# Kernel optimization log

Measured on AMD Instinct MI355X. Metric: run time of the kernel, lower is better.

## Reference

```python
import jax, jax.numpy as jnp
import numpy as np

EPS = 1e-5
HID = 32
FUSED = 33 * 33 * 33  # 35937


def _subnet(x, gamma, beta, W1, b1, W2, b2, W3, b3):
    # BatchNorm1d in training mode: batch mean / biased variance
    mu = jnp.mean(x, axis=0)
    var = jnp.mean((x - mu) ** 2, axis=0)
    xn = (x - mu) / jnp.sqrt(var + EPS) * gamma + beta
    h = jax.nn.relu(xn @ W1 + b1)
    h = jax.nn.relu(h @ W2 + b2)
    return jax.nn.relu(h @ W3 + b3)


def _subnet_params(key, in_dim):
    ks = jax.random.split(key, 6)
    s_in = 1.0 / np.sqrt(in_dim)
    s_h = 1.0 / np.sqrt(HID)
    return dict(
        gamma=jnp.ones((in_dim,), jnp.float32),
        beta=jnp.zeros((in_dim,), jnp.float32),
        W1=jax.random.uniform(ks[0], (in_dim, HID), jnp.float32, -s_in, s_in),
        b1=jax.random.uniform(ks[1], (HID,), jnp.float32, -s_in, s_in),
        W2=jax.random.uniform(ks[2], (HID, HID), jnp.float32, -s_h, s_h),
        b2=jax.random.uniform(ks[3], (HID,), jnp.float32, -s_h, s_h),
        W3=jax.random.uniform(ks[4], (HID, HID), jnp.float32, -s_h, s_h),
        b3=jax.random.uniform(ks[5], (HID,), jnp.float32, -s_h, s_h),
    )


def setup_inputs() -> dict:
    key = jax.random.key(0)
    ks = jax.random.split(key, 10)
    B = 8192
    inp = {
        'US_x': jax.random.normal(ks[0], (B, 1024), jnp.float32),
        'CDFI_x': jax.random.normal(ks[1], (B, 1024), jnp.float32),
        'marker_x': jax.random.normal(ks[2], (B, 10), jnp.float32),
    }
    for pref, k, d in (('us', ks[3], 1024), ('cd', ks[4], 1024), ('mk', ks[5], 10)):
        for n, v in _subnet_params(k, d).items():
            inp[f'{pref}_{n}'] = v
    s1 = 1.0 / np.sqrt(FUSED)
    s2 = 1.0 / np.sqrt(33)
    inp['Wf1'] = jax.random.uniform(ks[6], (FUSED, 33), jnp.float32, -s1, s1)
    inp['bf1'] = jax.random.uniform(ks[7], (33,), jnp.float32, -s1, s1)
    inp['Wf2'] = jax.random.uniform(ks[8], (33, 5), jnp.float32, -s2, s2)
    inp['bf2'] = jax.random.uniform(ks[9], (5,), jnp.float32, -s2, s2)
    return inp


def reference(US_x, CDFI_x, marker_x,
              us_gamma, us_beta, us_W1, us_b1, us_W2, us_b2, us_W3, us_b3,
              cd_gamma, cd_beta, cd_W1, cd_b1, cd_W2, cd_b2, cd_W3, cd_b3,
              mk_gamma, mk_beta, mk_W1, mk_b1, mk_W2, mk_b2, mk_W3, mk_b3,
              Wf1, bf1, Wf2, bf2):
    B = US_x.shape[0]
    us_h = _subnet(US_x, us_gamma, us_beta, us_W1, us_b1, us_W2, us_b2, us_W3, us_b3)
    cd_h = _subnet(CDFI_x, cd_gamma, cd_beta, cd_W1, cd_b1, cd_W2, cd_b2, cd_W3, cd_b3)
    mk_h = _subnet(marker_x, mk_gamma, mk_beta, mk_W1, mk_b1, mk_W2, mk_b2, mk_W3, mk_b3)
    ones = jnp.ones((B, 1), jnp.float32)
    us1 = jnp.concatenate([ones, us_h], axis=1)   # [B,33]
    cd1 = jnp.concatenate([ones, cd_h], axis=1)   # [B,33]
    mk1 = jnp.concatenate([ones, mk_h], axis=1)   # [B,33]
    # fused[b,k,j,i] = mk1[b,k] * cd1[b,j] * us1[b,i]; flattened row-major
    fused = jnp.einsum('bk,bj,bi->bkji', mk1, cd1, us1).reshape(B, FUSED)
    h = jax.nn.relu(fused @ Wf1 + bf1)
    return jax.nn.sigmoid(h @ Wf2 + bf2)
```

## Files before the change

kernel.cpp:

```cpp
#include <hip/hip_runtime.h>
#include <hip/hip_bf16.h>
#include <math.h>

typedef __hip_bfloat16 bf16;
typedef __attribute__((ext_vector_type(4))) float f32x4;
typedef __attribute__((ext_vector_type(8))) short s16x8;

#define NB 8192
#define KP 1152
#define NP 1152
#define NKT 18
#define SBLK 256

struct SubP {
    const float* x; const float* gamma; const float* beta;
    const float* W1; const float* b1; const float* W2; const float* b2;
    const float* W3; const float* b3;
    float* sum; float* sumsq; float* a; float* b1p; float* hout;
    int F;
};
struct SubP3 { SubP s[3]; };

__global__ void __launch_bounds__(256) stats3_kernel(SubP3 P) {
    const SubP p = P.s[blockIdx.z];
    int t = threadIdx.x;
    int blk = blockIdx.x;
    int row0 = blk * 32;
    if (p.F == 1024) {
        f32x4 s = {0.f, 0.f, 0.f, 0.f}, s2 = {0.f, 0.f, 0.f, 0.f};
        const float* xp = p.x + (size_t)row0 * 1024 + t * 4;
        #pragma unroll 8
        for (int r = 0; r < 32; r++) {
            f32x4 v = *(const f32x4*)(xp + (size_t)r * 1024);
            s += v; s2 += v * v;
        }
        int f = t * 4;
        *(f32x4*)&p.sum[(size_t)blk * 2048 + f]   = s;
        *(f32x4*)&p.sumsq[(size_t)blk * 2048 + f] = s2;
    } else {
        __shared__ float ls[16], ls2[16];
        if (t < 16) { ls[t] = 0.f; ls2[t] = 0.f; }
        __syncthreads();
        int F = p.F;
        for (int idx = t; idx < 32 * F; idx += 256) {
            float v = p.x[(size_t)row0 * F + idx];
            int f = idx % 10;
            atomicAdd(&ls[f], v);
            atomicAdd(&ls2[f], v * v);
        }
        __syncthreads();
        if (t < F) {
            p.sum[(size_t)blk * 2048 + t]   = ls[t];
            p.sumsq[(size_t)blk * 2048 + t] = ls2[t];
        }
    }
}

__global__ void prep3_kernel(SubP3 P) {
    const SubP p = P.s[blockIdx.y];
    int f0 = blockIdx.x * 32;
    if (f0 >= p.F) return;
    int t = threadIdx.x;
    __shared__ float c_sh[32];
    __shared__ float red[8][33];
    __shared__ float rs[8][33], rs2[8][33];
    int fc = p.F - f0; if (fc > 32) fc = 32;
    int fi = t & 31, g = t >> 5;
    {
        float s = 0.f, s2 = 0.f;
        if (fi < fc) {
            for (int blk = g; blk < SBLK; blk += 8) {
                s  += p.sum[(size_t)blk * 2048 + f0 + fi];
                s2 += p.sumsq[(size_t)blk * 2048 + f0 + fi];
            }
        }
        rs[g][fi] = s; rs2[g][fi] = s2;
    }
    __syncthreads();
    if (t < 32) {
        float c = 0.f;
        if (t < fc) {
            float sm = 0.f, sq = 0.f;
            #pragma unroll
            for (int gg = 0; gg < 8; gg++) { sm += rs[gg][t]; sq += rs2[gg][t]; }
            int f = f0 + t;
            float mu  = sm * (1.f / 8192.f);
            float var = sq * (1.f / 8192.f) - mu * mu;
            float a = p.gamma[f] * rsqrtf(var + 1e-5f);
            p.a[f] = a;
            c = p.beta[f] - mu * a;
        }
        c_sh[t] = c;
    }
    __syncthreads();
    int h = t & 31; g = t >> 5;
    float s = 0.f;
    for (int fi2 = g; fi2 < fc; fi2 += 8)
        s += c_sh[fi2] * p.W1[(size_t)(f0 + fi2) * 32 + h];
    red[g][h] = s;
    __syncthreads();
    if (t < 32) {
        float tot = 0.f;
        #pragma unroll
        for (int gg = 0; gg < 8; gg++) tot += red[gg][t];
        atomicAdd(&p.b1p[t], tot);
    }
}

__global__ void __launch_bounds__(256) subnet3_kernel(SubP3 P) {
    const SubP p = P.s[blockIdx.y];
    const int F = p.F;
    __shared__ float smem[8832];
    float* Red = smem;
    float* H1  = smem + 3456;
    float* W23 = smem + 4608;
    float* H2  = smem;

    int t = threadIdx.x;
    int row0 = blockIdx.x * 32;
    int kg = t >> 6;
    int lane = t & 63;
    int hg = lane & 7, h0 = hg * 4;
    int rg = (lane >> 3) & 3;
    int ks = lane >> 5;

    float acc[4][8] = {};

    if (F == 1024) {
        float* Xt = smem;
        float* Wt = smem + 4224;
        int xr = t >> 3, xc = (t & 7) * 16;
        int wk = t >> 1, wh = (t & 1) * 16;
        const float* xbase = p.x + (size_t)row0 * 1024;
        f32x4 xp[4], wp[4]; float av;
        #pragma unroll
        for (int i = 0; i < 4; i++) xp[i] = *(const f32x4*)&xbase[(size_t)xr * 1024 + xc + i * 4];
        #pragma unroll
        for (int i = 0; i < 4; i++) wp[i] = *(const f32x4*)&p.W1[(size_t)wk * 32 + wh + i * 4];
        av = p.a[wk];
        int kb = (kg * 2 + ks) * 16;
        for (int c = 0; c < 8; c++) {
            __syncthreads();
            #pragma unroll
            for (int i = 0; i < 4; i++) *(f32x4*)&Xt[xr * 132 + xc + i * 4] = xp[i];
            #pragma unroll
            for (int i = 0; i < 4; i++) *(f32x4*)&Wt[wk * 36 + wh + i * 4] = wp[i] * av;
            if (c < 7) {
                int k0 = (c + 1) * 128;
                #pragma unroll
                for (int i = 0; i < 4; i++) xp[i] = *(const f32x4*)&xbase[(size_t)xr * 1024 + k0 + xc + i * 4];
                #pragma unroll
                for (int i = 0; i < 4; i++) wp[i] = *(const f32x4*)&p.W1[(size_t)(k0 + wk) * 32 + wh + i * 4];
                av = p.a[k0 + wk];
            }
            __syncthreads();
            #pragma unroll
            for (int s = 0; s < 4; s++) {
                int kk = kb + s * 4;
                f32x4 wv[4], xv[8];
                #pragma unroll
                for (int j = 0; j < 4; j++)  wv[j]  = *(const f32x4*)&Wt[(kk + j) * 36 + h0];
                #pragma unroll
                for (int ri = 0; ri < 8; ri++) xv[ri] = *(const f32x4*)&Xt[(rg + 4 * ri) * 132 + kk];
                #pragma unroll
                for (int j = 0; j < 4; j++)
                    #pragma unroll
                    for (int hi = 0; hi < 4; hi++) {
                        float w = wv[j][hi];
                        #pragma unroll
                        for (int ri = 0; ri < 8; ri++)
                            acc[hi][ri] = fmaf(w, xv[ri][j], acc[hi][ri]);
                    }
            }
        }
    } else {
        float* Xt = smem;
        float* Wt = smem + 2176;
        int kbase = (kg * 2 + ks) * 8;
        for (int k0 = 0; k0 < F; k0 += 64) {
            int kc = F - k0; if (kc > 64) kc = 64;
            int kcp = (kc + 3) & ~3;
            __syncthreads();
            for (int idx = t; idx < 32 * kcp; idx += 256) {
                int r = idx / kcp, kk = idx - r * kcp;
                Xt[r * 68 + kk] = (kk < kc) ? p.x[(size_t)(row0 + r) * F + k0 + kk] : 0.f;
            }
            for (int idx = t; idx < kcp * 32; idx += 256) {
                int kk = idx >> 5, hh = idx & 31;
                Wt[kk * 36 + hh] = (kk < kc) ? p.a[k0 + kk] * p.W1[(size_t)(k0 + kk) * 32 + hh] : 0.f;
            }
            __syncthreads();
            #pragma unroll
            for (int s = 0; s < 2; s++) {
                int kk = kbase + s * 4;
                if (kk < kcp) {
                    f32x4 wv[4], xv[8];
                    #pragma unroll
                    for (int j = 0; j < 4; j++)  wv[j]  = *(const f32x4*)&Wt[(kk + j) * 36 + h0];
                    #pragma unroll
                    for (int ri = 0; ri < 8; ri++) xv[ri] = *(const f32x4*)&Xt[(rg + 4 * ri) * 68 + kk];
                    #pragma unroll
                    for (int j = 0; j < 4; j++)
                        #pragma unroll
                        for (int hi = 0; hi < 4; hi++) {
                            float w = wv[j][hi];
                            #pragma unroll
                            for (int ri = 0; ri < 8; ri++)
                                acc[hi][ri] = fmaf(w, xv[ri][j], acc[hi][ri]);
                        }
                }
            }
        }
    }
    #pragma unroll
    for (int hi = 0; hi < 4; hi++)
        #pragma unroll
        for (int ri = 0; ri < 8; ri++)
            acc[hi][ri] += __shfl_xor(acc[hi][ri], 32);
    __syncthreads();
    if (kg > 0 && ks == 0) {
        #pragma unroll
        for (int ri = 0; ri < 8; ri++) {
            int r = rg + 4 * ri;
            f32x4 v = {acc[0][ri], acc[1][ri], acc[2][ri], acc[3][ri]};
            *(f32x4*)&Red[(kg - 1) * 1152 + r * 36 + h0] = v;
        }
    }
    for (int idx = t; idx < 1024; idx += 256) W23[(idx >> 5) * 33 + (idx & 31)] = p.W2[idx];
    __syncthreads();
    if (kg == 0 && ks == 0) {
        f32x4 b;
        #pragma unroll
        for (int hi = 0; hi < 4; hi++) b[hi] = p.b1[h0 + hi] + p.b1p[h0 + hi];
        #pragma unroll
        for (int ri = 0; ri < 8; ri++) {
            int r = rg + 4 * ri;
            f32x4 v = {acc[0][ri], acc[1][ri], acc[2][ri], acc[3][ri]};
            #pragma unroll
            for (int pp = 0; pp < 3; pp++)
                v += *(const f32x4*)&Red[pp * 1152 + r * 36 + h0];
            v += b;
            #pragma unroll
            for (int hi = 0; hi < 4; hi++)
                H1[r * 36 + h0 + hi] = fmaxf(v[hi], 0.f);
        }
    }
    __syncthreads();
    int h = t & 31, rq = t >> 5;
    {
        float a2[4] = {};
        for (int q = 0; q < 32; q++) {
            float w = W23[q * 33 + h];
            #pragma unroll
            for (int i = 0; i < 4; i++) a2[i] += H1[(rq * 4 + i) * 36 + q] * w;
        }
        float bv = p.b2[h];
        #pragma unroll
        for (int i = 0; i < 4; i++) H2[(rq * 4 + i) * 36 + h] = fmaxf(a2[i] + bv, 0.f);
    }
    __syncthreads();
    for (int idx = t; idx < 1024; idx += 256) W23[(idx >> 5) * 33 + (idx & 31)] = p.W3[idx];
    __syncthreads();
    {
        float a3[4] = {};
        for (int q = 0; q < 32; q++) {
            float w = W23[q * 33 + h];
            #pragma unroll
            for (int i = 0; i < 4; i++) a3[i] += H2[(rq * 4 + i) * 36 + q] * w;
        }
        float bv = p.b3[h];
        #pragma unroll
        for (int i = 0; i < 4; i++)
            p.hout[(size_t)(row0 + rq * 4 + i) * 32 + h] = fmaxf(a3[i] + bv, 0.f);
    }
}

__global__ void __launch_bounds__(256) build_both(const float* __restrict__ mk_h,
                           const float* __restrict__ us_h,
                           bf16* __restrict__ p1,
                           const float* __restrict__ Wf1, bf16* __restrict__ W2t) {
    int blk = blockIdx.x;
    int t = threadIdx.x;
    if (blk < NB / 4) {
        int r = t >> 6, lane = t & 63;
        int b = blk * 4 + r;
        __shared__ float mk1[4][34], us1[4][34];
        if (lane == 0) { mk1[r][0] = 1.f; us1[r][0] = 1.f; }
        if (lane < 32) mk1[r][lane + 1] = mk_h[(size_t)b * 32 + lane];
        else           us1[r][lane - 31] = us_h[(size_t)b * 32 + (lane - 32)];
        __syncthreads();
        #pragma unroll
        for (int c = 0; c < 3; c++) {
            int chunk = lane + 64 * c;
            if (chunk < 144) {
                int base = chunk * 8;
                s16x8 v;
                #pragma unroll
                for (int e = 0; e < 8; e++) {
                    int idx = base + e;
                    float val = 0.f;
                    if (idx < 1089) {
                        int k = idx / 33, i = idx - k * 33;
                        val = mk1[r][k] * us1[r][i];
                    }
                    __hip_bfloat16 hb = __float2bfloat16(val);
                    v[e] = *(short*)&hb;
                }
                *(s16x8*)(p1 + (size_t)b * KP + base) = v;
            }
        }
    } else {
        int kj = blk - NB / 4;
        int k = kj / 33, j = kj - k * 33;
        __shared__ float tile[1089];
        const float* src = Wf1 + (size_t)k * 35937 + (size_t)j * 1089;
        for (int idx = t; idx < 1089; idx += 256) tile[idx] = src[idx];
        __syncthreads();
        for (int idx = t; idx < 1089; idx += 256) {
            int o = idx / 33, i = idx - o * 33;
            W2t[(size_t)(j * 33 + o) * KP + k * 33 + i] = __float2bfloat16(tile[i * 33 + o]);
        }
        if (k == 0) {
            bf16 z = __float2bfloat16(0.f);
            for (int idx = t; idx < 33 * 63; idx += 256) {
                int o = idx / 63, kkp = 1089 + idx - o * 63;
                W2t[(size_t)(j * 33 + o) * KP + kkp] = z;
            }
        }
    }
}

__global__ void __launch_bounds__(512) gemm_kernel(const bf16* __restrict__ A,
                                                   const bf16* __restrict__ Bt,
                                                   bf16* __restrict__ S) {
    __shared__ __align__(16) bf16 As[2][256 * 64];
    __shared__ __align__(16) bf16 Bs[2][192 * 64];
    int t = threadIdx.x;
    int wv = t >> 6, lane = t & 63;
    int m0 = blockIdx.x * 256;
    int n0 = blockIdx.y * 144;
    int fr = lane & 15;
    int q  = lane >> 4;
    int lr8 = lane >> 3;
    int sslot = (lane & 7) ^ lr8;

    const bf16* Ag = A  + (size_t)(m0 + wv * 32 + lr8) * KP + sslot * 8;
    const bf16* Bg = Bt + (size_t)(n0 + wv * 24 + lr8) * KP + sslot * 8;

    f32x4 acc[2][9] = {};

    auto stageA = [&](int buf, int T) {
        bf16* Ad = &As[buf][wv * 32 * 64];
        const bf16* s = Ag + T * 64;
        #pragma unroll
        for (int i = 0; i < 4; i++)
            __builtin_amdgcn_global_load_lds(
                (const __attribute__((address_space(1))) void*)(s + (size_t)i * 8 * KP),
                (__attribute__((address_space(3))) void*)(Ad + i * 512), 16, 0, 0);
    };
    auto stageB = [&](int buf, int T) {
        bf16* Bd = &Bs[buf][wv * 24 * 64];
        const bf16* s = Bg + T * 64;
        #pragma unroll
        for (int c = 0; c < 3; c++)
            __builtin_amdgcn_global_load_lds(
                (const __attribute__((address_space(1))) void*)(s + (size_t)c * 8 * KP),
                (__attribute__((address_space(3))) void*)(Bd + c * 512), 16, 0, 0);
    };

    stageA(0, 0);
    stageB(0, 0);

    for (int T = 0; T < NKT; T++) {
        int b = T & 1;
        const bf16* Ab = &As[b][0];
        const bf16* Bb = &Bs[b][0];
        if (T < NKT - 1) {
            stageA(b ^ 1, T + 1);
            asm volatile("s_waitcnt vmcnt(4)" ::: "memory");
        } else {
            asm volatile("s_waitcnt vmcnt(0)" ::: "memory");
        }
        __builtin_amdgcn_s_barrier();
        asm volatile("" ::: "memory");
        {
            int sl = (q ^ (fr & 7)) * 8;
            s16x8 af0 = *(const s16x8*)(Ab + (wv * 32 + fr) * 64 + sl);
            s16x8 af1 = *(const s16x8*)(Ab + (wv * 32 + 16 + fr) * 64 + sl);
            s16x8 bfv[9];
            #pragma unroll
            for (int n2 = 0; n2 < 9; n2++)
                bfv[n2] = *(const s16x8*)(Bb + (n2 * 16 + fr) * 64 + sl);
            __builtin_amdgcn_s_setprio(1);
            #pragma unroll
            for (int n2 = 0; n2 < 9; n2++) {
                acc[0][n2] = __builtin_amdgcn_mfma_f32_16x16x32_bf16(af0, bfv[n2], acc[0][n2], 0, 0, 0);
                acc[1][n2] = __builtin_amdgcn_mfma_f32_16x16x32_bf16(af1, bfv[n2], acc[1][n2], 0, 0, 0);
            }
            __builtin_amdgcn_s_setprio(0);
        }
        if (T < NKT - 1) stageB(b ^ 1, T + 1);
        {
            int sl = ((4 + q) ^ (fr & 7)) * 8;
            s16x8 af0 = *(const s16x8*)(Ab + (wv * 32 + fr) * 64 + sl);
            s16x8 af1 = *(const s16x8*)(Ab + (wv * 32 + 16 + fr) * 64 + sl);
            s16x8 bfv[9];
            #pragma unroll
            for (int n2 = 0; n2 < 9; n2++)
                bfv[n2] = *(const s16x8*)(Bb + (n2 * 16 + fr) * 64 + sl);
            __builtin_amdgcn_s_setprio(1);
            #pragma unroll
            for (int n2 = 0; n2 < 9; n2++) {
                acc[0][n2] = __builtin_amdgcn_mfma_f32_16x16x32_bf16(af0, bfv[n2], acc[0][n2], 0, 0, 0);
                acc[1][n2] = __builtin_amdgcn_mfma_f32_16x16x32_bf16(af1, bfv[n2], acc[1][n2], 0, 0, 0);
            }
            __builtin_amdgcn_s_setprio(0);
        }
        asm volatile("s_waitcnt lgkmcnt(0)" ::: "memory");
        __builtin_amdgcn_sched_barrier(0);
        __builtin_amdgcn_s_barrier();
        asm volatile("" ::: "memory");
    }

    int col = lane & 15, rowg = (lane >> 4) * 4;
    #pragma unroll
    for (int mt = 0; mt < 2; mt++)
        #pragma unroll
        for (int n2 = 0; n2 < 9; n2++)
            #pragma unroll
            for (int r = 0; r < 4; r++) {
                int gr = m0 + wv * 32 + mt * 16 + rowg + r;
                int gc = n0 + n2 * 16 + col;
                S[(size_t)gr * NP + gc] = __float2bfloat16(acc[mt][n2][r]);
            }
}

__global__ void __launch_bounds__(256) epilogue_kernel(const bf16* __restrict__ S,
                                const float* __restrict__ cd_h,
                                const float* __restrict__ bf1, const float* __restrict__ Wf2,
                                const float* __restrict__ bf2, float* __restrict__ out) {
    int w = threadIdx.x >> 6;
    int lane = threadIdx.x & 63;
    int b = blockIdx.x * 4 + w;
    __shared__ __align__(16) unsigned short Sl[4][1152];
    __shared__ float cdsh[4][33];
    __shared__ float hsh[4][40];
    const bf16* Srow = S + (size_t)b * NP;
    #pragma unroll
    for (int pass = 0; pass < 3; pass++) {
        int idx = lane + pass * 64;
        if (idx < 144)
            *(s16x8*)&Sl[w][idx * 8] = *(const s16x8*)(Srow + idx * 8);
    }
    if (lane == 0) cdsh[w][0] = 1.f;
    if (lane < 32) cdsh[w][lane + 1] = cd_h[(size_t)b * 32 + lane];
    __syncthreads();
    if (lane < 33) {
        float acc = bf1[lane];
        #pragma unroll 3
        for (int j = 0; j < 33; j++) {
            unsigned short sv = Sl[w][j * 33 + lane];
            acc += cdsh[w][j] * __bfloat162float(*(bf16*)&sv);
        }
        hsh[w][lane] = fmaxf(acc, 0.f);
    }
    __syncthreads();
    if (lane < 5) {
        float o = bf2[lane];
        for (int q = 0; q < 33; q++) o += hsh[w][q] * Wf2[q * 5 + lane];
        out[(size_t)b * 5 + lane] = 1.f / (1.f + expf(-o));
    }
}

extern "C" void kernel_launch(void* const* d_in, const int* in_sizes, int n_in,
                              void* d_out, int out_size, void* d_ws, size_t ws_size,
                              hipStream_t stream) {
    const float* US_x     = (const float*)d_in[0];
    const float* CDFI_x   = (const float*)d_in[1];
    const float* marker_x = (const float*)d_in[2];
    const float* Wf1      = (const float*)d_in[27];
    const float* bf1      = (const float*)d_in[28];
    const float* Wf2      = (const float*)d_in[29];
    const float* bf2      = (const float*)d_in[30];
    float* out = (float*)d_out;

    char* ws = (char*)d_ws;
    size_t off = 0;
    auto alloc = [&](size_t bytes) -> void* {
        void* p = ws + off;
        off = (off + bytes + 255) & ~(size_t)255;
        return p;
    };

    float* b1p_buf  = (float*)alloc(3 * 128 * sizeof(float));
    float* pstat    = (float*)alloc((size_t)3 * SBLK * 2048 * sizeof(float));
    float* a_buf[3], *h_buf[3];
    for (int i = 0; i < 3; i++) {
        a_buf[i] = (float*)alloc(1024 * 4);
        h_buf[i] = (float*)alloc((size_t)NB * 32 * 4);
    }
    bf16*  p1   = (bf16*)alloc((size_t)NB * KP * 2);
    bf16*  W2t  = (bf16*)alloc((size_t)NP * KP * 2);
    bf16*  S    = (bf16*)alloc((size_t)NB * NP * 2);

    SubP3 P;
    const float* xs[3] = {US_x, CDFI_x, marker_x};
    int Fs[3] = {1024, 1024, 10};
    for (int i = 0; i < 3; i++) {
        int base = 3 + i * 8;
        P.s[i].x     = xs[i];
        P.s[i].gamma = (const float*)d_in[base + 0];
        P.s[i].beta  = (const float*)d_in[base + 1];
        P.s[i].W1    = (const float*)d_in[base + 2];
        P.s[i].b1    = (const float*)d_in[base + 3];
        P.s[i].W2    = (const float*)d_in[base + 4];
        P.s[i].b2    = (const float*)d_in[base + 5];
        P.s[i].W3    = (const float*)d_in[base + 6];
        P.s[i].b3    = (const float*)d_in[base + 7];
        P.s[i].sum   = pstat + (size_t)i * SBLK * 2048;
        P.s[i].sumsq = pstat + (size_t)i * SBLK * 2048 + 1024;
        P.s[i].b1p   = b1p_buf + i * 128;
        P.s[i].a     = a_buf[i];
        P.s[i].hout  = h_buf[i];
        P.s[i].F     = Fs[i];
    }

    float* us_h = h_buf[0];
    float* cd_h = h_buf[1];
    float* mk_h = h_buf[2];

    hipMemsetAsync(b1p_buf, 0, 3 * 128 * sizeof(float), stream);

    stats3_kernel<<<dim3(SBLK, 1, 3), 256, 0, stream>>>(P);
    prep3_kernel<<<dim3(32, 3), 256, 0, stream>>>(P);
    subnet3_kernel<<<dim3(256, 3), 256, 0, stream>>>(P);

    build_both<<<NB / 4 + 1089, 256, 0, stream>>>(mk_h, us_h, p1, Wf1, W2t);

    gemm_kernel<<<dim3(NB / 256, NP / 144), 512, 0, stream>>>(p1, W2t, S);

    epilogue_kernel<<<NB / 4, 256, 0, stream>>>(S, cd_h, bf1, Wf2, bf2, out);
}
```

Baseline: 246.4 us.

## Use bf16 MFMA for subnet first layer with pre-scaled transposed W1

The prep kernel now writes a transposed, BN-scale-folded bf16 copy of W1 for the 1024-wide subnets. The subnet kernel stages X (converted to bf16) and that W1 copy into swizzled LDS and runs the first-layer matmul with 16x16x32 bf16 MFMA instructions, replacing the fp32 FMA loop. It also reorganizes the cross-wave reduction. This removes scalar FMA work but lowers the precision of the first layer to bf16 inputs.

```diff
diff --git a/kernel.cpp b/kernel.cpp
--- a/kernel.cpp
+++ b/kernel.cpp
@@ -17,6 +17,7 @@
     const float* W1; const float* b1; const float* W2; const float* b2;
     const float* W3; const float* b3;
     float* sum; float* sumsq; float* a; float* b1p; float* hout;
+    bf16* w1t;
     int F;
 };
 struct SubP3 { SubP s[3]; };
@@ -62,6 +63,7 @@
     if (f0 >= p.F) return;
     int t = threadIdx.x;
     __shared__ float c_sh[32];
+    __shared__ float ash[32];
     __shared__ float red[8][33];
     __shared__ float rs[8][33], rs2[8][33];
     int fc = p.F - f0; if (fc > 32) fc = 32;
@@ -78,7 +80,7 @@
     }
     __syncthreads();
     if (t < 32) {
-        float c = 0.f;
+        float c = 0.f, av = 0.f;
         if (t < fc) {
             float sm = 0.f, sq = 0.f;
             #pragma unroll
@@ -86,11 +88,11 @@
             int f = f0 + t;
             float mu  = sm * (1.f / 8192.f);
             float var = sq * (1.f / 8192.f) - mu * mu;
-            float a = p.gamma[f] * rsqrtf(var + 1e-5f);
-            p.a[f] = a;
-            c = p.beta[f] - mu * a;
-        }
-        c_sh[t] = c;
+            av = p.gamma[f] * rsqrtf(var + 1e-5f);
+            p.a[f] = av;
+            c = p.beta[f] - mu * av;
+        }
+        c_sh[t] = c; ash[t] = av;
     }
     __syncthreads();
     int h = t & 31; g = t >> 5;
@@ -105,12 +107,19 @@
         for (int gg = 0; gg < 8; gg++) tot += red[gg][t];
         atomicAdd(&p.b1p[t], tot);
     }
+    if (p.F == 1024) {
+        for (int idx = t; idx < 1024; idx += 256) {
+            int kk = idx >> 5, hh = idx & 31;
+            p.w1t[(size_t)hh * 1024 + f0 + kk] =
+                __float2bfloat16(ash[kk] * p.W1[(size_t)(f0 + kk) * 32 + hh]);
+        }
+    }
 }
 
 __global__ void __launch_bounds__(256) subnet3_kernel(SubP3 P) {
     const SubP p = P.s[blockIdx.y];
     const int F = p.F;
-    __shared__ float smem[8832];
+    __shared__ float smem[9760];
     float* Red = smem;
     float* H1  = smem + 3456;
     float* W23 = smem + 4608;
@@ -124,58 +133,105 @@
     int rg = (lane >> 3) & 3;
     int ks = lane >> 5;
 
-    float acc[4][8] = {};
-
     if (F == 1024) {
-        float* Xt = smem;
-        float* Wt = smem + 4224;
+        bf16* Xl = (bf16*)(smem + 5664);
+        bf16* Wl = (bf16*)(smem + 7712);
         int xr = t >> 3, xc = (t & 7) * 16;
-        int wk = t >> 1, wh = (t & 1) * 16;
-        const float* xbase = p.x + (size_t)row0 * 1024;
-        f32x4 xp[4], wp[4]; float av;
-        #pragma unroll
-        for (int i = 0; i < 4; i++) xp[i] = *(const f32x4*)&xbase[(size_t)xr * 1024 + xc + i * 4];
-        #pragma unroll
-        for (int i = 0; i < 4; i++) wp[i] = *(const f32x4*)&p.W1[(size_t)wk * 32 + wh + i * 4];
-        av = p.a[wk];
-        int kb = (kg * 2 + ks) * 16;
+        int sw = xr & 7;
+        int s0 = ((t & 7) * 2) ^ sw, s1 = ((t & 7) * 2 + 1) ^ sw;
+        const float* xbase = p.x + (size_t)(row0 + xr) * 1024 + xc;
+        const bf16*  wbase = p.w1t + (size_t)xr * 1024 + xc;
+        f32x4 xp[4]; s16x8 wp0, wp1;
+        #pragma unroll
+        for (int i = 0; i < 4; i++) xp[i] = *(const f32x4*)(xbase + i * 4);
+        wp0 = *(const s16x8*)(wbase);
+        wp1 = *(const s16x8*)(wbase + 8);
+
+        f32x4 acc[2][2] = {};
+        int fr = lane & 15, qq = lane >> 4;
+        int rsw0 = fr & 7;
+
         for (int c = 0; c < 8; c++) {
-            __syncthreads();
-            #pragma unroll
-            for (int i = 0; i < 4; i++) *(f32x4*)&Xt[xr * 132 + xc + i * 4] = xp[i];
-            #pragma unroll
-            for (int i = 0; i < 4; i++) *(f32x4*)&Wt[wk * 36 + wh + i * 4] = wp[i] * av;
+            __builtin_amdgcn_s_barrier();
+            asm volatile("" ::: "memory");
+            {
+                s16x8 v0, v1;
+                #pragma unroll
+                for (int i = 0; i < 2; i++)
+                    #pragma unroll
+                    for (int e = 0; e < 4; e++) {
+                        __hip_bfloat16 hb = __float2bfloat16(xp[i][e]);
+                        v0[i * 4 + e] = *(short*)&hb;
+                    }
+                #pragma unroll
+                for (int i = 0; i < 2; i++)
+                    #pragma unroll
+                    for (int e = 0; e < 4; e++) {
+                        __hip_bfloat16 hb = __float2bfloat16(xp[2 + i][e]);
+                        v1[i * 4 + e] = *(short*)&hb;
+                    }
+                *(s16x8*)((char*)Xl + xr * 256 + s0 * 16) = v0;
+                *(s16x8*)((char*)Xl + xr * 256 + s1 * 16) = v1;
+                *(s16x8*)((char*)Wl + xr * 256 + s0 * 16) = wp0;
+                *(s16x8*)((char*)Wl + xr * 256 + s1 * 16) = wp1;
+            }
             if (c < 7) {
                 int k0 = (c + 1) * 128;
                 #pragma unroll
-                for (int i = 0; i < 4; i++) xp[i] = *(const f32x4*)&xbase[(size_t)xr * 1024 + k0 + xc + i * 4];
-                #pragma unroll
-                for (int i = 0; i < 4; i++) wp[i] = *(const f32x4*)&p.W1[(size_t)(k0 + wk) * 32 + wh + i * 4];
-                av = p.a[k0 + wk];
-            }
-            __syncthreads();
-            #pragma unroll
-            for (int s = 0; s < 4; s++) {
-                int kk = kb + s * 4;
-                f32x4 wv[4], xv[8];
-                #pragma unroll
-                for (int j = 0; j < 4; j++)  wv[j]  = *(const f32x4*)&Wt[(kk + j) * 36 + h0];
-                #pragma unroll
-                for (int ri = 0; ri < 8; ri++) xv[ri] = *(const f32x4*)&Xt[(rg + 4 * ri) * 132 + kk];
-                #pragma unroll
-                for (int j = 0; j < 4; j++)
+                for (int i = 0; i < 4; i++) xp[i] = *(const f32x4*)(xbase + k0 + i * 4);
+                wp0 = *(const s16x8*)(wbase + k0);
+                wp1 = *(const s16x8*)(wbase + k0 + 8);
+            }
+            asm volatile("s_waitcnt lgkmcnt(0)" ::: "memory");
+            __builtin_amdgcn_sched_barrier(0);
+            __builtin_amdgcn_s_barrier();
+            asm volatile("" ::: "memory");
+            {
+                int sx = kg * 4 + qq;
+                int sl = (sx ^ rsw0) * 16;
+                s16x8 a0 = *(const s16x8*)((char*)Xl + fr * 256 + sl);
+                s16x8 a1 = *(const s16x8*)((char*)Xl + (16 + fr) * 256 + sl);
+                s16x8 b0 = *(const s16x8*)((char*)Wl + fr * 256 + sl);
+                s16x8 b1 = *(const s16x8*)((char*)Wl + (16 + fr) * 256 + sl);
+                acc[0][0] = __builtin_amdgcn_mfma_f32_16x16x32_bf16(a0, b0, acc[0][0], 0, 0, 0);
+                acc[0][1] = __builtin_amdgcn_mfma_f32_16x16x32_bf16(a0, b1, acc[0][1], 0, 0, 0);
+                acc[1][0] = __builtin_amdgcn_mfma_f32_16x16x32_bf16(a1, b0, acc[1][0], 0, 0, 0);
+                acc[1][1] = __builtin_amdgcn_mfma_f32_16x16x32_bf16(a1, b1, acc[1][1], 0, 0, 0);
+            }
+        }
+        int col = lane & 15, rowg = (lane >> 4) * 4;
+        if (kg > 0) {
+            #pragma unroll
+            for (int m = 0; m < 2; m++)
+                #pragma unroll
+                for (int n = 0; n < 2; n++)
                     #pragma unroll
-                    for (int hi = 0; hi < 4; hi++) {
-                        float w = wv[j][hi];
+                    for (int r = 0; r < 4; r++)
+                        Red[(kg - 1) * 1152 + (m * 16 + rowg + r) * 36 + n * 16 + col] = acc[m][n][r];
+        }
+        __syncthreads();
+        if (kg == 0) {
+            #pragma unroll
+            for (int m = 0; m < 2; m++)
+                #pragma unroll
+                for (int n = 0; n < 2; n++) {
+                    int cc = n * 16 + col;
+                    float bv = p.b1[cc] + p.b1p[cc];
+                    #pragma unroll
+                    for (int r = 0; r < 4; r++) {
+                        int rr = m * 16 + rowg + r;
+                        float v = acc[m][n][r] + bv;
                         #pragma unroll
-                        for (int ri = 0; ri < 8; ri++)
-                            acc[hi][ri] = fmaf(w, xv[ri][j], acc[hi][ri]);
+                        for (int pp = 0; pp < 3; pp++)
+                            v += Red[pp * 1152 + rr * 36 + cc];
+                        H1[rr * 36 + cc] = fmaxf(v, 0.f);
                     }
-            }
+                }
         }
     } else {
         float* Xt = smem;
         float* Wt = smem + 2176;
+        float acc[4][8] = {};
         int kbase = (kg * 2 + ks) * 8;
         for (int k0 = 0; k0 < F; k0 += 64) {
             int kc = F - k0; if (kc > 64) kc = 64;
@@ -211,40 +267,40 @@
                 }
             }
         }
-    }
-    #pragma unroll
-    for (int hi = 0; hi < 4; hi++)
-        #pragma unroll
-        for (int ri = 0; ri < 8; ri++)
-            acc[hi][ri] += __shfl_xor(acc[hi][ri], 32);
-    __syncthreads();
-    if (kg > 0 && ks == 0) {
-        #pragma unroll
-        for (int ri = 0; ri < 8; ri++) {
-            int r = rg + 4 * ri;
-            f32x4 v = {acc[0][ri], acc[1][ri], acc[2][ri], acc[3][ri]};
-            *(f32x4*)&Red[(kg - 1) * 1152 + r * 36 + h0] = v;
+        #pragma unroll
+        for (int hi = 0; hi < 4; hi++)
+            #pragma unroll
+            for (int ri = 0; ri < 8; ri++)
+                acc[hi][ri] += __shfl_xor(acc[hi][ri], 32);
+        __syncthreads();
+        if (kg > 0 && ks == 0) {
+            #pragma unroll
+            for (int ri = 0; ri < 8; ri++) {
+                int r = rg + 4 * ri;
+                f32x4 v = {acc[0][ri], acc[1][ri], acc[2][ri], acc[3][ri]};
+                *(f32x4*)&Red[(kg - 1) * 1152 + r * 36 + h0] = v;
+            }
+        }
+        __syncthreads();
+        if (kg == 0 && ks == 0) {
+            f32x4 b;
+            #pragma unroll
+            for (int hi = 0; hi < 4; hi++) b[hi] = p.b1[h0 + hi] + p.b1p[h0 + hi];
+            #pragma unroll
+            for (int ri = 0; ri < 8; ri++) {
+                int r = rg + 4 * ri;
+                f32x4 v = {acc[0][ri], acc[1][ri], acc[2][ri], acc[3][ri]};
+                #pragma unroll
+                for (int pp = 0; pp < 3; pp++)
+                    v += *(const f32x4*)&Red[pp * 1152 + r * 36 + h0];
+                v += b;
+                #pragma unroll
+                for (int hi = 0; hi < 4; hi++)
+                    H1[r * 36 + h0 + hi] = fmaxf(v[hi], 0.f);
+            }
         }
     }
     for (int idx = t; idx < 1024; idx += 256) W23[(idx >> 5) * 33 + (idx & 31)] = p.W2[idx];
-    __syncthreads();
-    if (kg == 0 && ks == 0) {
-        f32x4 b;
-        #pragma unroll
-        for (int hi = 0; hi < 4; hi++) b[hi] = p.b1[h0 + hi] + p.b1p[h0 + hi];
-        #pragma unroll
-        for (int ri = 0; ri < 8; ri++) {
-            int r = rg + 4 * ri;
-            f32x4 v = {acc[0][ri], acc[1][ri], acc[2][ri], acc[3][ri]};
-            #pragma unroll
-            for (int pp = 0; pp < 3; pp++)
-                v += *(const f32x4*)&Red[pp * 1152 + r * 36 + h0];
-            v += b;
-            #pragma unroll
-            for (int hi = 0; hi < 4; hi++)
-                H1[r * 36 + h0 + hi] = fmaxf(v[hi], 0.f);
-        }
-    }
     __syncthreads();
     int h = t & 31, rq = t >> 5;
     {
@@ -494,6 +550,7 @@
 
     float* b1p_buf  = (float*)alloc(3 * 128 * sizeof(float));
     float* pstat    = (float*)alloc((size_t)3 * SBLK * 2048 * sizeof(float));
+    bf16*  w1t_buf  = (bf16*)alloc((size_t)3 * 32 * 1024 * 2);
     float* a_buf[3], *h_buf[3];
     for (int i = 0; i < 3; i++) {
         a_buf[i] = (float*)alloc(1024 * 4);
@@ -522,6 +579,7 @@
         P.s[i].b1p   = b1p_buf + i * 128;
         P.s[i].a     = a_buf[i];
         P.s[i].hout  = h_buf[i];
+        P.s[i].w1t   = w1t_buf + (size_t)i * 32 * 1024;
         P.s[i].F     = Fs[i];
     }
 
```

New measurement: 235.5 us (median of 2 runs). -4.4%, faster.
